# Kernel tuning notes

Hardware: AMD Instinct MI355X
Metric: run time of the kernel (lower is better)

Reference implementation:

```python
import jax, jax.numpy as jnp
import numpy as np

NUM_EXPERTS = 8
NUM_SPIKE_EXPERTS = 2
TOTAL_EXPERTS = NUM_EXPERTS + NUM_SPIKE_EXPERTS
D_IN = 512
HIDDEN = 1024  # expert_dim == spike_expert_capacity
D_OUT = 256
TOP_K = 2


def setup_inputs() -> dict:
    key = jax.random.key(0)
    ks = jax.random.split(key, 8)
    B, T = 32768, 16
    x = jax.random.normal(ks[0], (B, D_IN), dtype=jnp.float32)
    spike_indicators = jax.random.uniform(ks[1], (B, T), dtype=jnp.float32)
    s = 0.02
    Wr = jax.random.normal(ks[2], (D_IN, TOTAL_EXPERTS), dtype=jnp.float32) * s
    br = jnp.zeros((TOTAL_EXPERTS,), dtype=jnp.float32)
    W1 = jax.random.normal(ks[3], (TOTAL_EXPERTS, D_IN, HIDDEN), dtype=jnp.float32) * s
    b1 = jnp.zeros((TOTAL_EXPERTS, HIDDEN), dtype=jnp.float32)
    W2 = jax.random.normal(ks[4], (TOTAL_EXPERTS, HIDDEN, D_OUT), dtype=jnp.float32) * s
    b2 = jnp.zeros((TOTAL_EXPERTS, D_OUT), dtype=jnp.float32)
    return {"x": x, "spike_indicators": spike_indicators, "Wr": Wr, "br": br,
            "W1": W1, "b1": b1, "W2": W2, "b2": b2}


def reference(x, spike_indicators, Wr, br, W1, b1, W2, b2):
    # Router logits (plain Dense router branch)
    router_logits = x @ Wr + br                                   # [B, E]
    # Spike-expert routing bias: mean spike indicator added to spike experts only
    spike_mask = jnp.concatenate(
        [jnp.zeros((NUM_EXPERTS,), x.dtype), jnp.ones((NUM_SPIKE_EXPERTS,), x.dtype)])
    avg_spike = jnp.mean(spike_indicators, axis=1, keepdims=True)  # [B, 1]
    adjusted = router_logits + avg_spike * spike_mask[None, :]
    router_probs = jax.nn.softmax(adjusted, axis=-1)               # [B, E]
    top_k_probs, top_k_idx = jax.lax.top_k(router_probs, TOP_K)    # [B, K]
    top_k_norm = top_k_probs / (jnp.sum(top_k_probs, axis=1, keepdims=True) + 1e-9)
    # All experts computed for all tokens (matches original dense loop)
    h = jax.nn.relu(jnp.einsum('bd,edh->beh', x, W1) + b1[None])   # [B, E, H]
    expert_stack = jnp.einsum('beh,eho->beo', h, W2) + b2[None]    # [B, E, O]
    # Gather top-k expert outputs per token and combine
    gathered = jnp.take_along_axis(expert_stack, top_k_idx[:, :, None], axis=1)  # [B, K, O]
    mixed = jnp.sum(gathered * top_k_norm[:, :, None], axis=1)     # [B, O]
    return mixed
```

## Files before the change

### kernel.cpp

```cpp
#include <hip/hip_runtime.h>
#include <hip/hip_bf16.h>
#include <stdint.h>
#include <stddef.h>

typedef __attribute__((ext_vector_type(8))) short short8;
typedef __attribute__((ext_vector_type(4))) float f32x4;

#define NTOK 32768
#define DIN 512
#define HID 1024
#define DOUT 256
#define NEXP 10

__device__ __forceinline__ unsigned short f2bf(float f) {
  unsigned int u = __float_as_uint(f);
  u += 0x7fffu + ((u >> 16) & 1u);
  return (unsigned short)(u >> 16);
}

__device__ __forceinline__ void gld16(void* lds, const void* g) {
  __builtin_amdgcn_global_load_lds(
      (const __attribute__((address_space(1))) unsigned int*)g,
      (__attribute__((address_space(3))) unsigned int*)lds, 16, 0, 0);
}

__global__ void k_transpose_wr(const float* __restrict__ wr, float* __restrict__ wrt) {
  for (int i = threadIdx.x; i < DIN * NEXP; i += 256) {
    int d = i / NEXP, e = i % NEXP;
    wrt[e * DIN + d] = wr[i];
  }
}

__global__ __launch_bounds__(256) void k_transpose_conv(
    const float* __restrict__ in, unsigned short* __restrict__ out, int R, int C) {
  __shared__ unsigned short tile[64][72];
  int tid = threadIdx.x;
  const float* ip = in + ((size_t)blockIdx.z * R + blockIdx.y * 64) * C + blockIdx.x * 64;
  int r = tid >> 2, c0 = (tid & 3) * 16;
  const float* p = ip + (size_t)r * C + c0;
#pragma unroll
  for (int j = 0; j < 16; j += 4) {
    float4 v = *(const float4*)(p + j);
    tile[r][c0 + j + 0] = f2bf(v.x);
    tile[r][c0 + j + 1] = f2bf(v.y);
    tile[r][c0 + j + 2] = f2bf(v.z);
    tile[r][c0 + j + 3] = f2bf(v.w);
  }
  __syncthreads();
  unsigned short* op = out + ((size_t)blockIdx.z * C + blockIdx.x * 64) * R + blockIdx.y * 64;
  int c = tid >> 2, r0 = (tid & 3) * 16;
  unsigned short* q = op + (size_t)c * R + r0;
  union { short8 v; unsigned short u[8]; } t0, t1;
#pragma unroll
  for (int j = 0; j < 8; j++) { t0.u[j] = tile[r0 + j][c]; t1.u[j] = tile[r0 + 8 + j][c]; }
  *(short8*)(q) = t0.v;
  *(short8*)(q + 8) = t1.v;
}

__global__ __launch_bounds__(256) void k_router(
    const float* __restrict__ x, const float* __restrict__ spike,
    const float* __restrict__ wrt, const float* __restrict__ br,
    unsigned short* __restrict__ xb, int* __restrict__ cnt,
    int* __restrict__ tok, float* __restrict__ wgt) {
  __shared__ int s_i0[64], s_i1[64];
  __shared__ float s_w0[64], s_w1[64];
  __shared__ int hist[NEXP], base_[NEXP], loc[NEXP];
  int tid = threadIdx.x, wave = tid >> 6, lane = tid & 63;
  if (tid < NEXP) { hist[tid] = 0; loc[tid] = 0; }
  __syncthreads();
  for (int t = 0; t < 16; t++) {
    int slot = wave * 16 + t;
    int b = blockIdx.x * 64 + slot;
    const float* xr = x + (size_t)b * DIN;
    float xv[8];
#pragma unroll
    for (int k = 0; k < 8; k++) xv[k] = xr[lane + 64 * k];
    unsigned short* xo = xb + (size_t)b * DIN;
#pragma unroll
    for (int k = 0; k < 8; k++) xo[lane + 64 * k] = f2bf(xv[k]);
    float lg[NEXP];
#pragma unroll
    for (int e = 0; e < NEXP; e++) {
      const float* w = wrt + e * DIN;
      float s = 0.f;
#pragma unroll
      for (int k = 0; k < 8; k++) s += xv[k] * w[lane + 64 * k];
      lg[e] = s;
    }
#pragma unroll
    for (int off = 32; off > 0; off >>= 1) {
#pragma unroll
      for (int e = 0; e < NEXP; e++) lg[e] += __shfl_xor(lg[e], off);
    }
    float sv = spike[(size_t)b * 16 + (lane & 15)];
    sv += __shfl_xor(sv, 8); sv += __shfl_xor(sv, 4);
    sv += __shfl_xor(sv, 2); sv += __shfl_xor(sv, 1);
    float avg = sv * 0.0625f;
#pragma unroll
    for (int e = 0; e < NEXP; e++) lg[e] += br[e];
    lg[8] += avg; lg[9] += avg;
    float mx = lg[0];
#pragma unroll
    for (int e = 1; e < NEXP; e++) mx = fmaxf(mx, lg[e]);
    float p[NEXP], ps = 0.f;
#pragma unroll
    for (int e = 0; e < NEXP; e++) { p[e] = __expf(lg[e] - mx); ps += p[e]; }
    int i0 = 0; float p0 = p[0];
#pragma unroll
    for (int e = 1; e < NEXP; e++) if (p[e] > p0) { p0 = p[e]; i0 = e; }
    float p1 = -1.f; int i1 = 0;
#pragma unroll
    for (int e = 0; e < NEXP; e++) if (e != i0 && p[e] > p1) { p1 = p[e]; i1 = e; }
    float inv = 1.f / (p0 + p1 + ps * 1e-9f);
    if (lane == 0) {
      s_i0[slot] = i0; s_i1[slot] = i1;
      s_w0[slot] = p0 * inv; s_w1[slot] = p1 * inv;
      atomicAdd(&hist[i0], 1); atomicAdd(&hist[i1], 1);
    }
  }
  __syncthreads();
  if (tid < NEXP) base_[tid] = atomicAdd(&cnt[tid], hist[tid]);
  __syncthreads();
  if (tid < 64) {
    int b = blockIdx.x * 64 + tid;
    int i0 = s_i0[tid], i1 = s_i1[tid];
    int s0 = base_[i0] + atomicAdd(&loc[i0], 1);
    tok[i0 * NTOK + s0] = b; wgt[i0 * NTOK + s0] = s_w0[tid];
    int s1 = base_[i1] + atomicAdd(&loc[i1], 1);
    tok[i1 * NTOK + s1] = b; wgt[i1 * NTOK + s1] = s_w1[tid];
  }
}

__global__ __launch_bounds__(256, 2) void k_moe(
    const unsigned short* __restrict__ xb, const unsigned short* __restrict__ w1t,
    const unsigned short* __restrict__ w2t, const float* __restrict__ b1,
    const float* __restrict__ b2, const int* __restrict__ cnt,
    const int* __restrict__ tok, const float* __restrict__ wgt,
    float* __restrict__ out) {
  int e = blockIdx.y;
  int n = cnt[e];
  int tile = blockIdx.x;
  if (tile * 64 >= n) return;
  __shared__ unsigned short xa[64 * 64];
  __shared__ unsigned short b1s[128 * 64];
  __shared__ unsigned short b2s[256 * 64];
  __shared__ unsigned short hs[64 * 128];
  __shared__ int stok[64];
  __shared__ float swgt[64];
  int tid = threadIdx.x;
  if (tid < 64) {
    int idx = tile * 64 + tid;
    bool v = idx < n;
    stok[tid] = v ? tok[e * NTOK + idx] : 0;
    swgt[tid] = v ? wgt[e * NTOK + idx] : 0.f;
  }
  __syncthreads();
  int wave = tid >> 6, lane = tid & 63, quad = lane >> 4, l16 = lane & 15;
  int wm = wave & 1, wn = wave >> 1;
  int srow = tid >> 3;
  int c8 = (tid & 7) ^ (srow & 7);
  const unsigned short* gx0 = xb + (size_t)stok[srow] * DIN + c8 * 8;
  const unsigned short* gx1 = xb + (size_t)stok[32 + srow] * DIN + c8 * 8;
  const unsigned short* w1e = w1t + (size_t)e * HID * DIN;
  const unsigned short* w2e = w2t + (size_t)e * DOUT * HID;
  const unsigned short* gb1 = w1e + (size_t)srow * DIN + c8 * 8;
  const unsigned short* gb2 = w2e + (size_t)srow * HID + c8 * 8;
  int ra0 = wm * 32 + l16, ra1 = ra0 + 16;
  int rh0 = wn * 64 + l16;
  int ro0 = wn * 128 + l16;
  f32x4 acc2[2][8];
#pragma unroll
  for (int nt = 0; nt < 8; nt++) {
    float bv = b2[e * DOUT + wn * 128 + nt * 16 + l16];
    acc2[0][nt] = (f32x4){bv, bv, bv, bv};
    acc2[1][nt] = (f32x4){bv, bv, bv, bv};
  }
  for (int hc = 0; hc < 8; hc++) {
    f32x4 acc1[2][4];
#pragma unroll
    for (int nt = 0; nt < 4; nt++) {
      float bv = b1[e * HID + hc * 128 + wn * 64 + nt * 16 + l16];
      acc1[0][nt] = (f32x4){bv, bv, bv, bv};
      acc1[1][nt] = (f32x4){bv, bv, bv, bv};
    }
    for (int ks = 0; ks < 8; ks++) {
      __syncthreads();
      gld16(xa + (size_t)tid * 8, gx0 + ks * 64);
      gld16(xa + ((size_t)tid + 256) * 8, gx1 + ks * 64);
#pragma unroll
      for (int s = 0; s < 4; s++)
        gld16(b1s + ((size_t)s * 256 + tid) * 8,
              gb1 + (size_t)hc * 128 * DIN + (size_t)s * 32 * DIN + ks * 64);
      __syncthreads();
#pragma unroll
      for (int ki2 = 0; ki2 < 2; ki2++) {
        int cq = ki2 * 4 + quad;
        short8 af[2], bf[4];
        af[0] = *(const short8*)(xa + (ra0 * 8 + (cq ^ (ra0 & 7))) * 8);
        af[1] = *(const short8*)(xa + (ra1 * 8 + (cq ^ (ra1 & 7))) * 8);
#pragma unroll
        for (int nt = 0; nt < 4; nt++) {
          int r = rh0 + nt * 16;
          bf[nt] = *(const short8*)(b1s + (r * 8 + (cq ^ (r & 7))) * 8);
        }
#pragma unroll
        for (int mt = 0; mt < 2; mt++)
#pragma unroll
          for (int nt = 0; nt < 4; nt++)
            acc1[mt][nt] = __builtin_amdgcn_mfma_f32_16x16x32_bf16(
                af[mt], bf[nt], acc1[mt][nt], 0, 0, 0);
      }
    }
#pragma unroll
    for (int mt = 0; mt < 2; mt++) {
#pragma unroll
      for (int nt = 0; nt < 4; nt++) {
        int col = wn * 64 + nt * 16 + l16;
        int c16 = col >> 3, co = col & 7;
#pragma unroll
        for (int r4 = 0; r4 < 4; r4++) {
          int r = wm * 32 + mt * 16 + quad * 4 + r4;
          float v = acc1[mt][nt][r4];
          hs[(r * 16 + (c16 ^ (r & 15))) * 8 + co] = f2bf(v > 0.f ? v : 0.f);
        }
      }
    }
    for (int k2 = 0; k2 < 2; k2++) {
      __syncthreads();
#pragma unroll
      for (int s = 0; s < 8; s++)
        gld16(b2s + ((size_t)s * 256 + tid) * 8,
              gb2 + (size_t)s * 32 * HID + hc * 128 + k2 * 64);
      __syncthreads();
#pragma unroll
      for (int ki2 = 0; ki2 < 2; ki2++) {
        int cq = ki2 * 4 + quad;
        int c16 = k2 * 8 + cq;
        short8 af[2], bf[8];
        af[0] = *(const short8*)(hs + (ra0 * 16 + (c16 ^ (ra0 & 15))) * 8);
        af[1] = *(const short8*)(hs + (ra1 * 16 + (c16 ^ (ra1 & 15))) * 8);
#pragma unroll
        for (int nt = 0; nt < 8; nt++) {
          int r = ro0 + nt * 16;
          bf[nt] = *(const short8*)(b2s + (r * 8 + (cq ^ (r & 7))) * 8);
        }
#pragma unroll
        for (int mt = 0; mt < 2; mt++)
#pragma unroll
          for (int nt = 0; nt < 8; nt++)
            acc2[mt][nt] = __builtin_amdgcn_mfma_f32_16x16x32_bf16(
                af[mt], bf[nt], acc2[mt][nt], 0, 0, 0);
      }
    }
  }
#pragma unroll
  for (int mt = 0; mt < 2; mt++) {
#pragma unroll
    for (int r4 = 0; r4 < 4; r4++) {
      int m = wm * 32 + mt * 16 + quad * 4 + r4;
      float wv = swgt[m];
      if (wv != 0.f) {
        int t = stok[m];
        float* op = out + (size_t)t * DOUT + wn * 128 + l16;
#pragma unroll
        for (int nt = 0; nt < 8; nt++)
          atomicAdd(op + nt * 16, acc2[mt][nt][r4] * wv);
      }
    }
  }
}

extern "C" void kernel_launch(void* const* d_in, const int* in_sizes, int n_in,
                              void* d_out, int out_size, void* d_ws, size_t ws_size,
                              hipStream_t stream) {
  (void)in_sizes; (void)n_in; (void)ws_size;
  const float* x     = (const float*)d_in[0];
  const float* spike = (const float*)d_in[1];
  const float* Wr    = (const float*)d_in[2];
  const float* br    = (const float*)d_in[3];
  const float* W1    = (const float*)d_in[4];
  const float* b1    = (const float*)d_in[5];
  const float* W2    = (const float*)d_in[6];
  const float* b2    = (const float*)d_in[7];
  float* out = (float*)d_out;
  char* ws = (char*)d_ws;
  unsigned short* xb  = (unsigned short*)(ws + 0);
  unsigned short* w1t = (unsigned short*)(ws + 33554432);
  unsigned short* w2t = (unsigned short*)(ws + 44040192);
  float* wrt          = (float*)(ws + 49283072);
  int*   cnt          = (int*)(ws + 49303552);
  int*   tok          = (int*)(ws + 49303616);
  float* wgt          = (float*)(ws + 50614336);

  hipMemsetAsync(cnt, 0, 64, stream);
  hipMemsetAsync(out, 0, (size_t)out_size * sizeof(float), stream);
  k_transpose_wr<<<1, 256, 0, stream>>>(Wr, wrt);
  k_transpose_conv<<<dim3(16, 8, 10), 256, 0, stream>>>(W1, w1t, DIN, HID);
  k_transpose_conv<<<dim3(4, 16, 10), 256, 0, stream>>>(W2, w2t, HID, DOUT);
  k_router<<<512, 256, 0, stream>>>(x, spike, wrt, br, xb, cnt, tok, wgt);
  k_moe<<<dim3(512, NEXP), 256, 0, stream>>>(xb, w1t, w2t, b1, b2, cnt, tok, wgt, out);
}
```

Measured before the change: 398.5 us.

## Double token tile to 128 with 8 waves and double-buffered LDS prefetch

The fused MoE kernel now processes 128 tokens per block with 512 threads instead of 64 tokens with 256 threads. Each block therefore loads W1 and W2 weight tiles once for twice as many tokens, roughly halving weight traffic per token. X, W1 and W2 staging move to double-buffered LDS. The next k-slice is prefetched via global_load_lds while the current slice feeds the MFMAs, which removes one barrier per step. The cost is a much larger LDS footprint (about 128 KB), allowing only one block per CU, and higher register pressure from larger accumulator tiles.

New measurement: 447.4 us. +12.3%, slower.

```diff
diff --git a/kernel.cpp b/kernel.cpp
--- a/kernel.cpp
+++ b/kernel.cpp
@@ -131,7 +131,7 @@
   }
 }
 
-__global__ __launch_bounds__(256, 2) void k_moe(
+__global__ __launch_bounds__(512, 2) void k_moe(
     const unsigned short* __restrict__ xb, const unsigned short* __restrict__ w1t,
     const unsigned short* __restrict__ w2t, const float* __restrict__ b1,
     const float* __restrict__ b2, const int* __restrict__ cnt,
@@ -140,16 +140,16 @@
   int e = blockIdx.y;
   int n = cnt[e];
   int tile = blockIdx.x;
-  if (tile * 64 >= n) return;
-  __shared__ unsigned short xa[64 * 64];
-  __shared__ unsigned short b1s[128 * 64];
-  __shared__ unsigned short b2s[256 * 64];
-  __shared__ unsigned short hs[64 * 128];
-  __shared__ int stok[64];
-  __shared__ float swgt[64];
+  if (tile * 128 >= n) return;
+  __shared__ unsigned short xa[2][8192];
+  __shared__ unsigned short b1h[2][8192];
+  __shared__ unsigned short b2h[2][8192];
+  __shared__ unsigned short hsh[16384];
+  __shared__ int stok[128];
+  __shared__ float swgt[128];
   int tid = threadIdx.x;
-  if (tid < 64) {
-    int idx = tile * 64 + tid;
+  if (tid < 128) {
+    int idx = tile * 128 + tid;
     bool v = idx < n;
     stok[tid] = v ? tok[e * NTOK + idx] : 0;
     swgt[tid] = v ? wgt[e * NTOK + idx] : 0.f;
@@ -158,116 +158,146 @@
   int wave = tid >> 6, lane = tid & 63, quad = lane >> 4, l16 = lane & 15;
   int wm = wave & 1, wn = wave >> 1;
   int srow = tid >> 3;
-  int c8 = (tid & 7) ^ (srow & 7);
-  const unsigned short* gx0 = xb + (size_t)stok[srow] * DIN + c8 * 8;
-  const unsigned short* gx1 = xb + (size_t)stok[32 + srow] * DIN + c8 * 8;
+  int sc8 = (tid & 7) ^ (srow & 7);
   const unsigned short* w1e = w1t + (size_t)e * HID * DIN;
   const unsigned short* w2e = w2t + (size_t)e * DOUT * HID;
-  const unsigned short* gb1 = w1e + (size_t)srow * DIN + c8 * 8;
-  const unsigned short* gb2 = w2e + (size_t)srow * HID + c8 * 8;
-  int ra0 = wm * 32 + l16, ra1 = ra0 + 16;
-  int rh0 = wn * 64 + l16;
-  int ro0 = wn * 128 + l16;
-  f32x4 acc2[2][8];
-#pragma unroll
-  for (int nt = 0; nt < 8; nt++) {
-    float bv = b2[e * DOUT + wn * 128 + nt * 16 + l16];
+  const unsigned short* gxA = xb + (size_t)stok[srow] * DIN + sc8 * 8;
+  const unsigned short* gxB = xb + (size_t)stok[64 + srow] * DIN + sc8 * 8;
+  const unsigned short* g1A = w1e + (size_t)srow * DIN + sc8 * 8;
+  const unsigned short* g2A = w2e + (size_t)(2 * srow + (sc8 >> 2)) * HID + (sc8 & 3) * 8;
+
+#define STAGE_X(nb, ks) do { \
+    gld16(&xa[nb][(unsigned)tid * 8], gxA + (ks) * 64); \
+    gld16(&xa[nb][((unsigned)tid + 512) * 8], gxB + (ks) * 64); } while (0)
+#define STAGE_W1(nb, hcv, ks) do { \
+    const unsigned short* p_ = g1A + (size_t)(hcv) * 128 * DIN + (ks) * 64; \
+    gld16(&b1h[nb][(unsigned)tid * 8], p_); \
+    gld16(&b1h[nb][((unsigned)tid + 512) * 8], p_ + 64 * DIN); } while (0)
+#define STAGE_W2(nb, hcv, k2) do { \
+    const unsigned short* p_ = g2A + (hcv) * 128 + (k2) * 32; \
+    gld16(&b2h[nb][(unsigned)tid * 8], p_); \
+    gld16(&b2h[nb][((unsigned)tid + 512) * 8], p_ + 128 * HID); } while (0)
+
+  f32x4 acc2[4][4];
+#pragma unroll
+  for (int nt = 0; nt < 4; nt++) {
+    float bv = b2[e * DOUT + wn * 64 + nt * 16 + l16];
     acc2[0][nt] = (f32x4){bv, bv, bv, bv};
     acc2[1][nt] = (f32x4){bv, bv, bv, bv};
-  }
+    acc2[2][nt] = (f32x4){bv, bv, bv, bv};
+    acc2[3][nt] = (f32x4){bv, bv, bv, bv};
+  }
+  STAGE_X(0, 0);
+  STAGE_W1(0, 0, 0);
+  __syncthreads();
+
   for (int hc = 0; hc < 8; hc++) {
-    f32x4 acc1[2][4];
-#pragma unroll
-    for (int nt = 0; nt < 4; nt++) {
-      float bv = b1[e * HID + hc * 128 + wn * 64 + nt * 16 + l16];
-      acc1[0][nt] = (f32x4){bv, bv, bv, bv};
-      acc1[1][nt] = (f32x4){bv, bv, bv, bv};
-    }
+    float bb0 = b1[e * HID + hc * 128 + wn * 32 + l16];
+    float bb1v = b1[e * HID + hc * 128 + wn * 32 + 16 + l16];
+    f32x4 acc1[4][2];
+#pragma unroll
+    for (int mt = 0; mt < 4; mt++) {
+      acc1[mt][0] = (f32x4){0.f, 0.f, 0.f, 0.f};
+      acc1[mt][1] = (f32x4){0.f, 0.f, 0.f, 0.f};
+    }
+#pragma unroll
     for (int ks = 0; ks < 8; ks++) {
-      __syncthreads();
-      gld16(xa + (size_t)tid * 8, gx0 + ks * 64);
-      gld16(xa + ((size_t)tid + 256) * 8, gx1 + ks * 64);
-#pragma unroll
-      for (int s = 0; s < 4; s++)
-        gld16(b1s + ((size_t)s * 256 + tid) * 8,
-              gb1 + (size_t)hc * 128 * DIN + (size_t)s * 32 * DIN + ks * 64);
-      __syncthreads();
+      if (ks < 7) {
+        STAGE_X((ks + 1) & 1, ks + 1);
+        STAGE_W1((ks + 1) & 1, hc, ks + 1);
+      } else {
+        int hcn = hc < 7 ? hc + 1 : 7;
+        STAGE_X(0, 0);
+        STAGE_W1(0, hcn, 0);
+      }
+      if (ks == 0) STAGE_W2(0, hc, 0);
+      if (ks == 1) STAGE_W2(1, hc, 1);
+      const unsigned short* xab = xa[ks & 1];
+      const unsigned short* w1b = b1h[ks & 1];
 #pragma unroll
       for (int ki2 = 0; ki2 < 2; ki2++) {
         int cq = ki2 * 4 + quad;
-        short8 af[2], bf[4];
-        af[0] = *(const short8*)(xa + (ra0 * 8 + (cq ^ (ra0 & 7))) * 8);
-        af[1] = *(const short8*)(xa + (ra1 * 8 + (cq ^ (ra1 & 7))) * 8);
-#pragma unroll
-        for (int nt = 0; nt < 4; nt++) {
-          int r = rh0 + nt * 16;
-          bf[nt] = *(const short8*)(b1s + (r * 8 + (cq ^ (r & 7))) * 8);
+        short8 af[4], bf[2];
+#pragma unroll
+        for (int mt = 0; mt < 4; mt++) {
+          int r = wm * 64 + mt * 16 + l16;
+          af[mt] = *(const short8*)(xab + ((unsigned)(r * 8 + (cq ^ (r & 7)))) * 8);
         }
 #pragma unroll
-        for (int mt = 0; mt < 2; mt++)
-#pragma unroll
-          for (int nt = 0; nt < 4; nt++)
+        for (int nt = 0; nt < 2; nt++) {
+          int r = wn * 32 + nt * 16 + l16;
+          bf[nt] = *(const short8*)(w1b + ((unsigned)(r * 8 + (cq ^ (r & 7)))) * 8);
+        }
+#pragma unroll
+        for (int mt = 0; mt < 4; mt++)
+#pragma unroll
+          for (int nt = 0; nt < 2; nt++)
             acc1[mt][nt] = __builtin_amdgcn_mfma_f32_16x16x32_bf16(
                 af[mt], bf[nt], acc1[mt][nt], 0, 0, 0);
       }
-    }
-#pragma unroll
-    for (int mt = 0; mt < 2; mt++) {
+      __syncthreads();
+    }
+#pragma unroll
+    for (int mt = 0; mt < 4; mt++) {
+#pragma unroll
+      for (int nt = 0; nt < 2; nt++) {
+        int col = wn * 32 + nt * 16 + l16;
+        int c16 = col >> 3, co = col & 7;
+        float bb = nt ? bb1v : bb0;
+#pragma unroll
+        for (int r4 = 0; r4 < 4; r4++) {
+          int r = wm * 64 + mt * 16 + quad * 4 + r4;
+          float v = acc1[mt][nt][r4] + bb;
+          hsh[((unsigned)(r * 16 + (c16 ^ (r & 15)))) * 8 + co] = f2bf(v > 0.f ? v : 0.f);
+        }
+      }
+    }
+    __syncthreads();
+#pragma unroll
+    for (int k2 = 0; k2 < 4; k2++) {
+      if (k2 == 1) STAGE_W2(0, hc, 2);
+      if (k2 == 2) STAGE_W2(1, hc, 3);
+      const unsigned short* b2b = b2h[k2 & 1];
+      short8 af[4], bf[4];
+      int c16 = k2 * 4 + quad;
+#pragma unroll
+      for (int mt = 0; mt < 4; mt++) {
+        int r = wm * 64 + mt * 16 + l16;
+        af[mt] = *(const short8*)(&hsh[((unsigned)(r * 16 + (c16 ^ (r & 15)))) * 8]);
+      }
 #pragma unroll
       for (int nt = 0; nt < 4; nt++) {
-        int col = wn * 64 + nt * 16 + l16;
-        int c16 = col >> 3, co = col & 7;
-#pragma unroll
-        for (int r4 = 0; r4 < 4; r4++) {
-          int r = wm * 32 + mt * 16 + quad * 4 + r4;
-          float v = acc1[mt][nt][r4];
-          hs[(r * 16 + (c16 ^ (r & 15))) * 8 + co] = f2bf(v > 0.f ? v : 0.f);
-        }
-      }
-    }
-    for (int k2 = 0; k2 < 2; k2++) {
+        int r = wn * 64 + nt * 16 + l16;
+        int inner = (((r & 1) << 2) | quad) ^ ((r >> 1) & 7);
+        bf[nt] = *(const short8*)(&b2b[((unsigned)((r >> 1) * 8 + inner)) * 8]);
+      }
+#pragma unroll
+      for (int mt = 0; mt < 4; mt++)
+#pragma unroll
+        for (int nt = 0; nt < 4; nt++)
+          acc2[mt][nt] = __builtin_amdgcn_mfma_f32_16x16x32_bf16(
+              af[mt], bf[nt], acc2[mt][nt], 0, 0, 0);
       __syncthreads();
-#pragma unroll
-      for (int s = 0; s < 8; s++)
-        gld16(b2s + ((size_t)s * 256 + tid) * 8,
-              gb2 + (size_t)s * 32 * HID + hc * 128 + k2 * 64);
-      __syncthreads();
-#pragma unroll
-      for (int ki2 = 0; ki2 < 2; ki2++) {
-        int cq = ki2 * 4 + quad;
-        int c16 = k2 * 8 + cq;
-        short8 af[2], bf[8];
-        af[0] = *(const short8*)(hs + (ra0 * 16 + (c16 ^ (ra0 & 15))) * 8);
-        af[1] = *(const short8*)(hs + (ra1 * 16 + (c16 ^ (ra1 & 15))) * 8);
-#pragma unroll
-        for (int nt = 0; nt < 8; nt++) {
-          int r = ro0 + nt * 16;
-          bf[nt] = *(const short8*)(b2s + (r * 8 + (cq ^ (r & 7))) * 8);
-        }
-#pragma unroll
-        for (int mt = 0; mt < 2; mt++)
-#pragma unroll
-          for (int nt = 0; nt < 8; nt++)
-            acc2[mt][nt] = __builtin_amdgcn_mfma_f32_16x16x32_bf16(
-                af[mt], bf[nt], acc2[mt][nt], 0, 0, 0);
-      }
-    }
-  }
-#pragma unroll
-  for (int mt = 0; mt < 2; mt++) {
+    }
+  }
+#pragma unroll
+  for (int mt = 0; mt < 4; mt++) {
 #pragma unroll
     for (int r4 = 0; r4 < 4; r4++) {
-      int m = wm * 32 + mt * 16 + quad * 4 + r4;
+      int m = wm * 64 + mt * 16 + quad * 4 + r4;
       float wv = swgt[m];
       if (wv != 0.f) {
         int t = stok[m];
-        float* op = out + (size_t)t * DOUT + wn * 128 + l16;
-#pragma unroll
-        for (int nt = 0; nt < 8; nt++)
+        float* op = out + (size_t)t * DOUT + wn * 64 + l16;
+#pragma unroll
+        for (int nt = 0; nt < 4; nt++)
           atomicAdd(op + nt * 16, acc2[mt][nt][r4] * wv);
       }
     }
   }
+#undef STAGE_X
+#undef STAGE_W1
+#undef STAGE_W2
 }
 
 extern "C" void kernel_launch(void* const* d_in, const int* in_sizes, int n_in,
@@ -298,5 +328,5 @@
   k_transpose_conv<<<dim3(16, 8, 10), 256, 0, stream>>>(W1, w1t, DIN, HID);
   k_transpose_conv<<<dim3(4, 16, 10), 256, 0, stream>>>(W2, w2t, HID, DOUT);
   k_router<<<512, 256, 0, stream>>>(x, spike, wrt, br, xb, cnt, tok, wgt);
-  k_moe<<<dim3(512, NEXP), 256, 0, stream>>>(xb, w1t, w2t, b1, b2, cnt, tok, wgt, out);
-}
+  k_moe<<<dim3(256, NEXP), 512, 0, stream>>>(xb, w1t, w2t, b1, b2, cnt, tok, wgt, out);
+}
```

## Fuse prep kernels into one launch and double-buffer MoE weight tile loads

Applied to the files above, without the earlier changes.

Merges the Wr transpose, the W1/W2 bf16 transpose-conversions, the output memset and the router into a single k_prep launch. The router reads Wr directly into registers and zeroes its slice of the output. In k_moe the separate LDS buffers become a double-buffered xa/wp pair, so the next x/W1/W2 tile is prefetched while MFMAs run on the current one, with one barrier per step instead of two. W2 tiles are rearranged into 32-column chunks with a new swizzle. The change cuts launch overhead and hides global-to-LDS latency, at the cost of trickier buffer-reuse ordering between phases.

After: 426.5 us. +7.0%, slower.

```diff
diff --git a/kernel.cpp b/kernel.cpp
--- a/kernel.cpp
+++ b/kernel.cpp
@@ -12,80 +12,112 @@
 #define DOUT 256
 #define NEXP 10
 
+#define TW1_BLOCKS 1280
+#define TW2_BLOCKS 640
+#define RT_BLOCKS  512
+
 __device__ __forceinline__ unsigned short f2bf(float f) {
   unsigned int u = __float_as_uint(f);
   u += 0x7fffu + ((u >> 16) & 1u);
   return (unsigned short)(u >> 16);
 }
 
+__device__ __forceinline__ unsigned long long pack4bf(float4 v) {
+  return (unsigned long long)f2bf(v.x) | ((unsigned long long)f2bf(v.y) << 16) |
+         ((unsigned long long)f2bf(v.z) << 32) | ((unsigned long long)f2bf(v.w) << 48);
+}
+
 __device__ __forceinline__ void gld16(void* lds, const void* g) {
   __builtin_amdgcn_global_load_lds(
       (const __attribute__((address_space(1))) unsigned int*)g,
       (__attribute__((address_space(3))) unsigned int*)lds, 16, 0, 0);
 }
 
-__global__ void k_transpose_wr(const float* __restrict__ wr, float* __restrict__ wrt) {
-  for (int i = threadIdx.x; i < DIN * NEXP; i += 256) {
-    int d = i / NEXP, e = i % NEXP;
-    wrt[e * DIN + d] = wr[i];
-  }
-}
-
-__global__ __launch_bounds__(256) void k_transpose_conv(
-    const float* __restrict__ in, unsigned short* __restrict__ out, int R, int C) {
-  __shared__ unsigned short tile[64][72];
+union PrepSmem {
+  unsigned short tile[64][72];
+  struct {
+    int i0[64]; int i1[64]; float w0[64]; float w1[64];
+    int hist[NEXP]; int base_[NEXP]; int loc[NEXP];
+  } rt;
+};
+
+__global__ __launch_bounds__(256) void k_prep(
+    const float* __restrict__ x, const float* __restrict__ spike,
+    const float* __restrict__ Wr, const float* __restrict__ br,
+    const float* __restrict__ W1, const float* __restrict__ W2,
+    unsigned short* __restrict__ xb, unsigned short* __restrict__ w1t,
+    unsigned short* __restrict__ w2t, int* __restrict__ cnt,
+    int* __restrict__ tok, float* __restrict__ wgt, float* __restrict__ out) {
+  __shared__ PrepSmem sm;
+  int bid = blockIdx.x;
   int tid = threadIdx.x;
-  const float* ip = in + ((size_t)blockIdx.z * R + blockIdx.y * 64) * C + blockIdx.x * 64;
-  int r = tid >> 2, c0 = (tid & 3) * 16;
-  const float* p = ip + (size_t)r * C + c0;
-#pragma unroll
-  for (int j = 0; j < 16; j += 4) {
-    float4 v = *(const float4*)(p + j);
-    tile[r][c0 + j + 0] = f2bf(v.x);
-    tile[r][c0 + j + 1] = f2bf(v.y);
-    tile[r][c0 + j + 2] = f2bf(v.z);
-    tile[r][c0 + j + 3] = f2bf(v.w);
-  }
+
+  if (bid < TW1_BLOCKS + TW2_BLOCKS) {
+    const float* in; unsigned short* outp; int R, C, bx, by, bz;
+    if (bid < TW1_BLOCKS) {
+      int r = bid; bz = r >> 7; r &= 127; by = r >> 4; bx = r & 15;
+      in = W1; outp = w1t; R = DIN; C = HID;
+    } else {
+      int r = bid - TW1_BLOCKS; bz = r >> 6; r &= 63; by = r >> 2; bx = r & 3;
+      in = W2; outp = w2t; R = HID; C = DOUT;
+    }
+    const float* ip = in + ((size_t)bz * R + by * 64) * C + bx * 64;
+    int rr = tid >> 2, c0 = (tid & 3) * 16;
+    const float* p = ip + (size_t)rr * C + c0;
+#pragma unroll
+    for (int j = 0; j < 16; j += 4) {
+      float4 v = *(const float4*)(p + j);
+      sm.tile[rr][c0 + j + 0] = f2bf(v.x);
+      sm.tile[rr][c0 + j + 1] = f2bf(v.y);
+      sm.tile[rr][c0 + j + 2] = f2bf(v.z);
+      sm.tile[rr][c0 + j + 3] = f2bf(v.w);
+    }
+    __syncthreads();
+    unsigned short* op = outp + ((size_t)bz * C + bx * 64) * R + by * 64;
+    int c = tid >> 2, r0 = (tid & 3) * 16;
+    unsigned short* q = op + (size_t)c * R + r0;
+    union { short8 v; unsigned short u[8]; } t0, t1;
+#pragma unroll
+    for (int j = 0; j < 8; j++) { t0.u[j] = sm.tile[r0 + j][c]; t1.u[j] = sm.tile[r0 + 8 + j][c]; }
+    *(short8*)(q) = t0.v;
+    *(short8*)(q + 8) = t1.v;
+    return;
+  }
+
+  int rb = bid - (TW1_BLOCKS + TW2_BLOCKS);
+  int wave = tid >> 6, lane = tid & 63;
+  {
+    float4 z = {0.f, 0.f, 0.f, 0.f};
+    float4* ob = (float4*)(out + (size_t)rb * 64 * DOUT);
+#pragma unroll
+    for (int i = 0; i < 16; i++) ob[i * 256 + tid] = z;
+  }
+  if (tid < NEXP) { sm.rt.hist[tid] = 0; sm.rt.loc[tid] = 0; }
   __syncthreads();
-  unsigned short* op = out + ((size_t)blockIdx.z * C + blockIdx.x * 64) * R + blockIdx.y * 64;
-  int c = tid >> 2, r0 = (tid & 3) * 16;
-  unsigned short* q = op + (size_t)c * R + r0;
-  union { short8 v; unsigned short u[8]; } t0, t1;
-#pragma unroll
-  for (int j = 0; j < 8; j++) { t0.u[j] = tile[r0 + j][c]; t1.u[j] = tile[r0 + 8 + j][c]; }
-  *(short8*)(q) = t0.v;
-  *(short8*)(q + 8) = t1.v;
-}
-
-__global__ __launch_bounds__(256) void k_router(
-    const float* __restrict__ x, const float* __restrict__ spike,
-    const float* __restrict__ wrt, const float* __restrict__ br,
-    unsigned short* __restrict__ xb, int* __restrict__ cnt,
-    int* __restrict__ tok, float* __restrict__ wgt) {
-  __shared__ int s_i0[64], s_i1[64];
-  __shared__ float s_w0[64], s_w1[64];
-  __shared__ int hist[NEXP], base_[NEXP], loc[NEXP];
-  int tid = threadIdx.x, wave = tid >> 6, lane = tid & 63;
-  if (tid < NEXP) { hist[tid] = 0; loc[tid] = 0; }
-  __syncthreads();
+  float4 wv[NEXP][2];
+  float brr[NEXP];
+#pragma unroll
+  for (int e = 0; e < NEXP; e++) {
+    brr[e] = br[e];
+#pragma unroll
+    for (int h = 0; h < 2; h++) {
+      int d0 = h * 256 + lane * 4;
+      wv[e][h] = (float4){Wr[(size_t)(d0 + 0) * NEXP + e], Wr[(size_t)(d0 + 1) * NEXP + e],
+                          Wr[(size_t)(d0 + 2) * NEXP + e], Wr[(size_t)(d0 + 3) * NEXP + e]};
+    }
+  }
   for (int t = 0; t < 16; t++) {
     int slot = wave * 16 + t;
-    int b = blockIdx.x * 64 + slot;
-    const float* xr = x + (size_t)b * DIN;
-    float xv[8];
-#pragma unroll
-    for (int k = 0; k < 8; k++) xv[k] = xr[lane + 64 * k];
-    unsigned short* xo = xb + (size_t)b * DIN;
-#pragma unroll
-    for (int k = 0; k < 8; k++) xo[lane + 64 * k] = f2bf(xv[k]);
+    int b = rb * 64 + slot;
+    const float4* xr4 = (const float4*)(x + (size_t)b * DIN);
+    float4 xv0 = xr4[lane], xv1 = xr4[64 + lane];
+    *(unsigned long long*)(xb + (size_t)b * DIN + lane * 4) = pack4bf(xv0);
+    *(unsigned long long*)(xb + (size_t)b * DIN + 256 + lane * 4) = pack4bf(xv1);
     float lg[NEXP];
 #pragma unroll
     for (int e = 0; e < NEXP; e++) {
-      const float* w = wrt + e * DIN;
-      float s = 0.f;
-#pragma unroll
-      for (int k = 0; k < 8; k++) s += xv[k] * w[lane + 64 * k];
-      lg[e] = s;
+      lg[e] = xv0.x * wv[e][0].x + xv0.y * wv[e][0].y + xv0.z * wv[e][0].z + xv0.w * wv[e][0].w +
+              xv1.x * wv[e][1].x + xv1.y * wv[e][1].y + xv1.z * wv[e][1].z + xv1.w * wv[e][1].w;
     }
 #pragma unroll
     for (int off = 32; off > 0; off >>= 1) {
@@ -97,7 +129,7 @@
     sv += __shfl_xor(sv, 2); sv += __shfl_xor(sv, 1);
     float avg = sv * 0.0625f;
 #pragma unroll
-    for (int e = 0; e < NEXP; e++) lg[e] += br[e];
+    for (int e = 0; e < NEXP; e++) lg[e] += brr[e];
     lg[8] += avg; lg[9] += avg;
     float mx = lg[0];
 #pragma unroll
@@ -113,21 +145,21 @@
     for (int e = 0; e < NEXP; e++) if (e != i0 && p[e] > p1) { p1 = p[e]; i1 = e; }
     float inv = 1.f / (p0 + p1 + ps * 1e-9f);
     if (lane == 0) {
-      s_i0[slot] = i0; s_i1[slot] = i1;
-      s_w0[slot] = p0 * inv; s_w1[slot] = p1 * inv;
-      atomicAdd(&hist[i0], 1); atomicAdd(&hist[i1], 1);
+      sm.rt.i0[slot] = i0; sm.rt.i1[slot] = i1;
+      sm.rt.w0[slot] = p0 * inv; sm.rt.w1[slot] = p1 * inv;
+      atomicAdd(&sm.rt.hist[i0], 1); atomicAdd(&sm.rt.hist[i1], 1);
     }
   }
   __syncthreads();
-  if (tid < NEXP) base_[tid] = atomicAdd(&cnt[tid], hist[tid]);
+  if (tid < NEXP) sm.rt.base_[tid] = atomicAdd(&cnt[tid], sm.rt.hist[tid]);
   __syncthreads();
   if (tid < 64) {
-    int b = blockIdx.x * 64 + tid;
-    int i0 = s_i0[tid], i1 = s_i1[tid];
-    int s0 = base_[i0] + atomicAdd(&loc[i0], 1);
-    tok[i0 * NTOK + s0] = b; wgt[i0 * NTOK + s0] = s_w0[tid];
-    int s1 = base_[i1] + atomicAdd(&loc[i1], 1);
-    tok[i1 * NTOK + s1] = b; wgt[i1 * NTOK + s1] = s_w1[tid];
+    int b = rb * 64 + tid;
+    int i0 = sm.rt.i0[tid], i1 = sm.rt.i1[tid];
+    int s0 = sm.rt.base_[i0] + atomicAdd(&sm.rt.loc[i0], 1);
+    tok[i0 * NTOK + s0] = b; wgt[i0 * NTOK + s0] = sm.rt.w0[tid];
+    int s1 = sm.rt.base_[i1] + atomicAdd(&sm.rt.loc[i1], 1);
+    tok[i1 * NTOK + s1] = b; wgt[i1 * NTOK + s1] = sm.rt.w1[tid];
   }
 }
 
@@ -141,10 +173,9 @@
   int n = cnt[e];
   int tile = blockIdx.x;
   if (tile * 64 >= n) return;
-  __shared__ unsigned short xa[64 * 64];
-  __shared__ unsigned short b1s[128 * 64];
-  __shared__ unsigned short b2s[256 * 64];
-  __shared__ unsigned short hs[64 * 128];
+  __shared__ unsigned short xa[2][4096];
+  __shared__ unsigned short wp[2][8192];
+  __shared__ unsigned short hs[8192];
   __shared__ int stok[64];
   __shared__ float swgt[64];
   int tid = threadIdx.x;
@@ -164,7 +195,7 @@
   const unsigned short* w1e = w1t + (size_t)e * HID * DIN;
   const unsigned short* w2e = w2t + (size_t)e * DOUT * HID;
   const unsigned short* gb1 = w1e + (size_t)srow * DIN + c8 * 8;
-  const unsigned short* gb2 = w2e + (size_t)srow * HID + c8 * 8;
+  const unsigned short* gb2 = w2e + (size_t)(2 * srow + (c8 >> 2)) * HID + (c8 & 3) * 8;
   int ra0 = wm * 32 + l16, ra1 = ra0 + 16;
   int rh0 = wn * 64 + l16;
   int ro0 = wn * 128 + l16;
@@ -175,6 +206,12 @@
     acc2[0][nt] = (f32x4){bv, bv, bv, bv};
     acc2[1][nt] = (f32x4){bv, bv, bv, bv};
   }
+  gld16(xa[0] + (size_t)tid * 8, gx0);
+  gld16(xa[0] + ((size_t)tid + 256) * 8, gx1);
+#pragma unroll
+  for (int s = 0; s < 4; s++)
+    gld16(wp[0] + ((size_t)s * 256 + tid) * 8, gb1 + (size_t)s * 32 * DIN);
+
   for (int hc = 0; hc < 8; hc++) {
     f32x4 acc1[2][4];
 #pragma unroll
@@ -183,25 +220,34 @@
       acc1[0][nt] = (f32x4){bv, bv, bv, bv};
       acc1[1][nt] = (f32x4){bv, bv, bv, bv};
     }
+#pragma unroll 1
     for (int ks = 0; ks < 8; ks++) {
       __syncthreads();
-      gld16(xa + (size_t)tid * 8, gx0 + ks * 64);
-      gld16(xa + ((size_t)tid + 256) * 8, gx1 + ks * 64);
-#pragma unroll
-      for (int s = 0; s < 4; s++)
-        gld16(b1s + ((size_t)s * 256 + tid) * 8,
-              gb1 + (size_t)hc * 128 * DIN + (size_t)s * 32 * DIN + ks * 64);
-      __syncthreads();
+      if (ks < 7) {
+        gld16(xa[(ks + 1) & 1] + (size_t)tid * 8, gx0 + (ks + 1) * 64);
+        gld16(xa[(ks + 1) & 1] + ((size_t)tid + 256) * 8, gx1 + (ks + 1) * 64);
+#pragma unroll
+        for (int s = 0; s < 4; s++)
+          gld16(wp[(ks + 1) & 1] + ((size_t)s * 256 + tid) * 8,
+                gb1 + (size_t)hc * 128 * DIN + (size_t)s * 32 * DIN + (ks + 1) * 64);
+      } else {
+#pragma unroll
+        for (int s = 0; s < 4; s++)
+          gld16(wp[0] + ((size_t)s * 256 + tid) * 8,
+                gb2 + (size_t)s * 64 * HID + hc * 128);
+      }
+      const unsigned short* xab = xa[ks & 1];
+      const unsigned short* w1b = wp[ks & 1];
 #pragma unroll
       for (int ki2 = 0; ki2 < 2; ki2++) {
         int cq = ki2 * 4 + quad;
         short8 af[2], bf[4];
-        af[0] = *(const short8*)(xa + (ra0 * 8 + (cq ^ (ra0 & 7))) * 8);
-        af[1] = *(const short8*)(xa + (ra1 * 8 + (cq ^ (ra1 & 7))) * 8);
+        af[0] = *(const short8*)(xab + (ra0 * 8 + (cq ^ (ra0 & 7))) * 8);
+        af[1] = *(const short8*)(xab + (ra1 * 8 + (cq ^ (ra1 & 7))) * 8);
 #pragma unroll
         for (int nt = 0; nt < 4; nt++) {
           int r = rh0 + nt * 16;
-          bf[nt] = *(const short8*)(b1s + (r * 8 + (cq ^ (r & 7))) * 8);
+          bf[nt] = *(const short8*)(w1b + (r * 8 + (cq ^ (r & 7))) * 8);
         }
 #pragma unroll
         for (int mt = 0; mt < 2; mt++)
@@ -225,32 +271,39 @@
         }
       }
     }
-    for (int k2 = 0; k2 < 2; k2++) {
+#pragma unroll 1
+    for (int k2 = 0; k2 < 4; k2++) {
       __syncthreads();
-#pragma unroll
-      for (int s = 0; s < 8; s++)
-        gld16(b2s + ((size_t)s * 256 + tid) * 8,
-              gb2 + (size_t)s * 32 * HID + hc * 128 + k2 * 64);
-      __syncthreads();
-#pragma unroll
-      for (int ki2 = 0; ki2 < 2; ki2++) {
-        int cq = ki2 * 4 + quad;
-        int c16 = k2 * 8 + cq;
-        short8 af[2], bf[8];
-        af[0] = *(const short8*)(hs + (ra0 * 16 + (c16 ^ (ra0 & 15))) * 8);
-        af[1] = *(const short8*)(hs + (ra1 * 16 + (c16 ^ (ra1 & 15))) * 8);
-#pragma unroll
-        for (int nt = 0; nt < 8; nt++) {
-          int r = ro0 + nt * 16;
-          bf[nt] = *(const short8*)(b2s + (r * 8 + (cq ^ (r & 7))) * 8);
-        }
-#pragma unroll
-        for (int mt = 0; mt < 2; mt++)
-#pragma unroll
-          for (int nt = 0; nt < 8; nt++)
-            acc2[mt][nt] = __builtin_amdgcn_mfma_f32_16x16x32_bf16(
-                af[mt], bf[nt], acc2[mt][nt], 0, 0, 0);
-      }
+      if (k2 < 3) {
+#pragma unroll
+        for (int s = 0; s < 4; s++)
+          gld16(wp[(k2 + 1) & 1] + ((size_t)s * 256 + tid) * 8,
+                gb2 + (size_t)s * 64 * HID + hc * 128 + (k2 + 1) * 32);
+      } else if (hc < 7) {
+        gld16(xa[0] + (size_t)tid * 8, gx0);
+        gld16(xa[0] + ((size_t)tid + 256) * 8, gx1);
+#pragma unroll
+        for (int s = 0; s < 4; s++)
+          gld16(wp[0] + ((size_t)s * 256 + tid) * 8,
+                gb1 + (size_t)(hc + 1) * 128 * DIN + (size_t)s * 32 * DIN);
+      }
+      const unsigned short* b2b = wp[k2 & 1];
+      int c16 = k2 * 4 + quad;
+      short8 af[2], bf[8];
+      af[0] = *(const short8*)(hs + (ra0 * 16 + (c16 ^ (ra0 & 15))) * 8);
+      af[1] = *(const short8*)(hs + (ra1 * 16 + (c16 ^ (ra1 & 15))) * 8);
+#pragma unroll
+      for (int nt = 0; nt < 8; nt++) {
+        int rr = ro0 + nt * 16;
+        int inner = (((rr & 1) << 2) | quad) ^ ((rr >> 1) & 7);
+        bf[nt] = *(const short8*)(b2b + ((rr >> 1) * 8 + inner) * 8);
+      }
+#pragma unroll
+      for (int mt = 0; mt < 2; mt++)
+#pragma unroll
+        for (int nt = 0; nt < 8; nt++)
+          acc2[mt][nt] = __builtin_amdgcn_mfma_f32_16x16x32_bf16(
+              af[mt], bf[nt], acc2[mt][nt], 0, 0, 0);
     }
   }
 #pragma unroll
@@ -273,7 +326,7 @@
 extern "C" void kernel_launch(void* const* d_in, const int* in_sizes, int n_in,
                               void* d_out, int out_size, void* d_ws, size_t ws_size,
                               hipStream_t stream) {
-  (void)in_sizes; (void)n_in; (void)ws_size;
+  (void)in_sizes; (void)n_in; (void)ws_size; (void)out_size;
   const float* x     = (const float*)d_in[0];
   const float* spike = (const float*)d_in[1];
   const float* Wr    = (const float*)d_in[2];
@@ -287,16 +340,12 @@
   unsigned short* xb  = (unsigned short*)(ws + 0);
   unsigned short* w1t = (unsigned short*)(ws + 33554432);
   unsigned short* w2t = (unsigned short*)(ws + 44040192);
-  float* wrt          = (float*)(ws + 49283072);
   int*   cnt          = (int*)(ws + 49303552);
   int*   tok          = (int*)(ws + 49303616);
   float* wgt          = (float*)(ws + 50614336);
 
   hipMemsetAsync(cnt, 0, 64, stream);
-  hipMemsetAsync(out, 0, (size_t)out_size * sizeof(float), stream);
-  k_transpose_wr<<<1, 256, 0, stream>>>(Wr, wrt);
-  k_transpose_conv<<<dim3(16, 8, 10), 256, 0, stream>>>(W1, w1t, DIN, HID);
-  k_transpose_conv<<<dim3(4, 16, 10), 256, 0, stream>>>(W2, w2t, HID, DOUT);
-  k_router<<<512, 256, 0, stream>>>(x, spike, wrt, br, xb, cnt, tok, wgt);
+  k_prep<<<TW1_BLOCKS + TW2_BLOCKS + RT_BLOCKS, 256, 0, stream>>>(
+      x, spike, Wr, br, W1, W2, xb, w1t, w2t, cnt, tok, wgt, out);
   k_moe<<<dim3(512, NEXP), 256, 0, stream>>>(xb, w1t, w2t, b1, b2, cnt, tok, wgt, out);
 }
```
